# Kernel optimization log

Hardware: AMD Instinct MI355X
Metric: run time of the kernel (lower is better)

Reference implementation:

```python
import jax, jax.numpy as jnp
import numpy as np

DIM = 1024
N_HEADS = 16
HEAD_DIM = DIM // N_HEADS


def setup_inputs() -> dict:
    key = jax.random.key(0)
    ks = jax.random.split(key, 5)
    s = 0.02
    return {
        "x": jax.random.normal(ks[0], (2, 2048, DIM), dtype=jnp.float32),
        "w_qkv": jax.random.normal(ks[1], (DIM, 3 * DIM), dtype=jnp.float32) * s,
        "b_qkv": jnp.zeros((3 * DIM,), dtype=jnp.float32),
        "w_proj": jax.random.normal(ks[2], (DIM, DIM), dtype=jnp.float32) * s,
        "b_proj": jnp.zeros((DIM,), dtype=jnp.float32),
    }


def reference(x, w_qkv, b_qkv, w_proj, b_proj):
    B, N, C = x.shape
    H, D = N_HEADS, HEAD_DIM
    qkv = x @ w_qkv + b_qkv                      # [B, N, 3C]
    qkv = qkv.reshape(B, N, 3, H, D)
    q = qkv[:, :, 0].transpose(0, 2, 1, 3)       # [B, H, N, D]
    k = qkv[:, :, 1].transpose(0, 2, 1, 3)
    v = qkv[:, :, 2].transpose(0, 2, 1, 3)
    scale = 1.0 / np.sqrt(D).astype(np.float32)
    attn = jnp.einsum('bhnd,bhmd->bhnm', q, k) * scale
    attn = jax.nn.softmax(attn, axis=-1)
    out = jnp.einsum('bhnm,bhmd->bhnd', attn, v)  # [B, H, N, D]
    out = out.transpose(0, 2, 1, 3).reshape(B, N, C)
    return out @ w_proj + b_proj
```

## Files before the change

kernel.cpp:

```cpp
#include <hip/hip_runtime.h>

#define DIM    1024
#define NHEADS 16
#define HDIM   64
#define BATCH  2
#define SEQ    2048
#define ROWS   (BATCH * SEQ)
#define KDIM   1024

typedef __attribute__((ext_vector_type(4))) float f32x4;
typedef __attribute__((ext_vector_type(16))) float f32x16;
typedef __attribute__((ext_vector_type(8))) short bf16x8;

__device__ inline unsigned short f2bf(float f) {
  return (unsigned short)((__float_as_uint(f) + 0x8000u) >> 16);
}
__device__ inline float bf2f(unsigned short h) {
  return __uint_as_float(((unsigned int)h) << 16);
}
__device__ inline void split2(float x, unsigned short& hi, unsigned short& lo) {
  hi = f2bf(x);
  lo = f2bf(x - bf2f(hi));
}
__device__ inline int key2(int r) { return (r & 3) ^ ((r >> 2) & 3); }
__device__ inline int key8(int r) { return (r & 7) ^ ((r >> 3) & 7); }

__device__ inline void gll16(const void* g, void* lds_base) {
  __builtin_amdgcn_global_load_lds(
      (const __attribute__((address_space(1))) void*)g,
      (__attribute__((address_space(3))) void*)lds_base, 16, 0, 0);
}
__device__ inline unsigned int cvtpk_bf16(float a, float b) {
  unsigned int r;
  asm("v_cvt_pk_bf16_f32 %0, %1, %2" : "=v"(r) : "v"(a), "v"(b));
  return r;
}
template <int N>
__device__ inline void vm_wait() {
  if constexpr (N == 0)      asm volatile("s_waitcnt vmcnt(0)" ::: "memory");
  else if constexpr (N == 4) asm volatile("s_waitcnt vmcnt(4)" ::: "memory");
  else if constexpr (N == 6) asm volatile("s_waitcnt vmcnt(6)" ::: "memory");
  else                       asm volatile("s_waitcnt vmcnt(8)" ::: "memory");
}

__global__ __launch_bounds__(256) void split_x_kernel(
    const float* __restrict__ x, ushort* __restrict__ Xh) {
  const int i = blockIdx.x * 256 + threadIdx.x;
  const float4 v = ((const float4*)x)[i];
  ushort4 h4;
  h4.x = f2bf(v.x);
  h4.y = f2bf(v.y);
  h4.z = f2bf(v.z);
  h4.w = f2bf(v.w);
  ((ushort4*)Xh)[i] = h4;
}

template <int Ndim, bool LO>
__global__ __launch_bounds__(256) void tsplit_w(const float* __restrict__ W,
                                                ushort* __restrict__ WTh,
                                                ushort* __restrict__ WTl) {
  __shared__ float Ls[64][68];
  const int t = threadIdx.x;
  const int n0 = blockIdx.x * 64, k0 = blockIdx.y * 64;
#pragma unroll
  for (int pass = 0; pass < 4; ++pass) {
    const int kk = pass * 16 + (t >> 4);
    const float4 v =
        *(const float4*)(W + (size_t)(k0 + kk) * Ndim + n0 + (t & 15) * 4);
    *(float4*)&Ls[kk][(t & 15) * 4] = v;
  }
  __syncthreads();
  const int nloc = t >> 2, kc = (t & 3) * 16;
#pragma unroll
  for (int j = 0; j < 4; ++j) {
    ushort4 h4, l4;
    split2(Ls[kc + j * 4 + 0][nloc], h4.x, l4.x);
    split2(Ls[kc + j * 4 + 1][nloc], h4.y, l4.y);
    split2(Ls[kc + j * 4 + 2][nloc], h4.z, l4.z);
    split2(Ls[kc + j * 4 + 3][nloc], h4.w, l4.w);
    const size_t off = (size_t)(n0 + nloc) * KDIM + k0 + kc + j * 4;
    *(ushort4*)(WTh + off) = h4;
    if (LO) *(ushort4*)(WTl + off) = l4;
  }
}

template <int NPROD, int MODE, bool PIPE3>
__global__ __launch_bounds__(256) void gemm_mfma(
    const ushort* __restrict__ Ahp, const ushort* __restrict__ Alp,
    const ushort* __restrict__ Bhp, const ushort* __restrict__ Blp,
    const float* __restrict__ bias, float* __restrict__ Cout,
    ushort* __restrict__ Qh, ushort* __restrict__ Kh,
    ushort* __restrict__ VTh, int Ndim) {
  constexpr int NPLANES = NPROD + 1;
  constexpr int CALLS = NPLANES * 2;
  constexpr int BUFE = NPLANES * 128 * 32;
  constexpr int NBUF = PIPE3 ? 3 : 2;
  __shared__ ushort lds[NBUF][BUFE];

  const int t = threadIdx.x, w = t >> 6, lane = t & 63;
  const int l15 = lane & 15, lg = lane >> 4;
  const int n0 = blockIdx.x * 128, m0 = blockIdx.y * 128;
  const int wr = (w >> 1) * 64;
  const int wc = (w & 1) * 64;

  const ushort* srcs[4];
  srcs[0] = Ahp + (size_t)m0 * KDIM;
  if constexpr (NPROD == 1) {
    srcs[1] = Bhp + (size_t)n0 * KDIM;
    srcs[2] = srcs[3] = srcs[1];
  } else {
    srcs[1] = Alp + (size_t)m0 * KDIM;
    srcs[2] = Bhp + (size_t)n0 * KDIM;
    srcs[3] = Blp + (size_t)n0 * KDIM;
  }

  f32x4 acc[4][4];
#pragma unroll
  for (int a = 0; a < 4; ++a)
#pragma unroll
    for (int bq = 0; bq < 4; ++bq) acc[a][bq] = (f32x4){0.f, 0.f, 0.f, 0.f};

  auto stage = [&](int bi, int k0) {
#pragma unroll
    for (int i = 0; i < CALLS; ++i) {
      const int cbase = (w * CALLS + i) * 64;
      const int c = cbase + lane;
      const int p = c >> 9, cc = c & 511, r = cc >> 2, s = cc & 3;
      const ushort* g = srcs[p] + (size_t)r * KDIM + k0 + ((s ^ key2(r)) << 3);
      gll16(g, (char*)&lds[bi][0] + cbase * 16);
    }
  };

  auto compute = [&](const ushort* L) {
    if constexpr (NPROD == 1) {
      bf16x8 af[4];
#pragma unroll
      for (int mt = 0; mt < 4; ++mt) {
        const int row = wr + mt * 16 + l15;
        af[mt] = *(const bf16x8*)&L[row * 32 + ((lg ^ key2(row)) << 3)];
      }
      if constexpr (PIPE3) __builtin_amdgcn_s_setprio(1);
#pragma unroll
      for (int nt = 0; nt < 4; ++nt) {
        const int row = wc + nt * 16 + l15;
        const bf16x8 bh_ =
            *(const bf16x8*)&L[4096 + row * 32 + ((lg ^ key2(row)) << 3)];
#pragma unroll
        for (int mt = 0; mt < 4; ++mt)
          acc[mt][nt] = __builtin_amdgcn_mfma_f32_16x16x32_bf16(
              af[mt], bh_, acc[mt][nt], 0, 0, 0);
      }
      if constexpr (PIPE3) __builtin_amdgcn_s_setprio(0);
    } else {
      bf16x8 af[4][2];
#pragma unroll
      for (int mt = 0; mt < 4; ++mt) {
        const int row = wr + mt * 16 + l15;
        const int off = row * 32 + ((lg ^ key2(row)) << 3);
        af[mt][0] = *(const bf16x8*)&L[off];
        af[mt][1] = *(const bf16x8*)&L[4096 + off];
      }
      if constexpr (PIPE3) __builtin_amdgcn_s_setprio(1);
#pragma unroll
      for (int nt = 0; nt < 4; ++nt) {
        const int row = wc + nt * 16 + l15;
        const int off = row * 32 + ((lg ^ key2(row)) << 3);
        const bf16x8 bh_ = *(const bf16x8*)&L[8192 + off];
#pragma unroll
        for (int mt = 0; mt < 4; ++mt) {
          acc[mt][nt] = __builtin_amdgcn_mfma_f32_16x16x32_bf16(
              af[mt][0], bh_, acc[mt][nt], 0, 0, 0);
          acc[mt][nt] = __builtin_amdgcn_mfma_f32_16x16x32_bf16(
              af[mt][1], bh_, acc[mt][nt], 0, 0, 0);
        }
        const bf16x8 bl_ = *(const bf16x8*)&L[12288 + off];
#pragma unroll
        for (int mt = 0; mt < 4; ++mt)
          acc[mt][nt] = __builtin_amdgcn_mfma_f32_16x16x32_bf16(
              af[mt][0], bl_, acc[mt][nt], 0, 0, 0);
      }
      if constexpr (PIPE3) __builtin_amdgcn_s_setprio(0);
    }
  };

  if constexpr (PIPE3) {
    constexpr int NSTEP = KDIM / 32;
    stage(0, 0);
    stage(1, 32);
    for (int it = 0; it < NSTEP; ++it) {
      if (it + 1 < NSTEP) vm_wait<CALLS>(); else vm_wait<0>();
      __builtin_amdgcn_s_barrier();
      __builtin_amdgcn_sched_barrier(0);
      if (it + 2 < NSTEP) stage((it + 2) % 3, (it + 2) * 32);
      compute(&lds[it % 3][0]);
    }
  } else {
    stage(0, 0);
    __syncthreads();
    for (int k0 = 0, it = 0; k0 < KDIM; k0 += 32, ++it) {
      const int cur = it & 1;
      if (k0 + 32 < KDIM) stage(cur ^ 1, k0 + 32);
      compute(&lds[cur][0]);
      __syncthreads();
    }
  }

  if constexpr (MODE == 0) {
#pragma unroll
    for (int nt = 0; nt < 4; ++nt) {
      const int col = n0 + wc + nt * 16 + l15;
      const float bv = bias[col];
#pragma unroll
      for (int mt = 0; mt < 4; ++mt) {
        const int row = m0 + wr + mt * 16 + lg * 4;
#pragma unroll
        for (int r = 0; r < 4; ++r)
          Cout[(size_t)(row + r) * Ndim + col] = acc[mt][nt][r] + bv;
      }
    }
  } else {
    const int sec = n0 >> 10;
#pragma unroll
    for (int nt = 0; nt < 4; ++nt) {
      const int col = n0 + wc + nt * 16 + l15;
      const float bv = bias[col];
      const int cw = col & 1023;
      if (sec == 0) {
#pragma unroll
        for (int mt = 0; mt < 4; ++mt) {
          const int row = m0 + wr + mt * 16 + lg * 4;
#pragma unroll
          for (int r = 0; r < 4; ++r)
            Qh[(size_t)(row + r) * DIM + cw] =
                f2bf((acc[mt][nt][r] + bv) * (0.125f * 1.44269504f));
        }
      } else if (sec == 1) {
#pragma unroll
        for (int mt = 0; mt < 4; ++mt) {
          const int row = m0 + wr + mt * 16 + lg * 4;
#pragma unroll
          for (int r = 0; r < 4; ++r)
            Kh[(size_t)(row + r) * DIM + cw] = f2bf(acc[mt][nt][r] + bv);
        }
      } else {
        const int h = cw >> 6, d = cw & 63;
#pragma unroll
        for (int mt = 0; mt < 4; ++mt) {
          const int grow = m0 + wr + mt * 16 + lg * 4;
          const int b = grow >> 11, n = grow & 2047;
          ushort4 v4;
          v4.x = f2bf(acc[mt][nt][0] + bv);
          v4.y = f2bf(acc[mt][nt][1] + bv);
          v4.z = f2bf(acc[mt][nt][2] + bv);
          v4.w = f2bf(acc[mt][nt][3] + bv);
          *(ushort4*)(VTh + ((size_t)(b * NHEADS + h) * HDIM + d) * SEQ + n) =
              v4;
        }
      }
    }
  }
}

__global__ __launch_bounds__(256) void attn_mfma32(
    const ushort* __restrict__ Qhp, const ushort* __restrict__ Khp,
    const ushort* __restrict__ VThp, ushort* __restrict__ AOh,
    ushort* __restrict__ AOl) {
  __shared__ ushort KV2[3][2 * 64 * 64];

  const int t = threadIdx.x, w = t >> 6, lane = t & 63;
  const int l31 = lane & 31, hi = lane >> 5;
  const int q0 = blockIdx.x * 128;
  const int bh = blockIdx.y, b = bh >> 4, h = bh & 15;

  bf16x8 qf[4];
  {
    const ushort* qp = Qhp +
        (size_t)(b * SEQ + q0 + w * 32 + l31) * DIM + h * HDIM + hi * 8;
    int4 qi[4];
#pragma unroll
    for (int j = 0; j < 4; ++j) qi[j] = *(const int4*)(qp + 16 * j);
#pragma unroll
    for (int j = 0; j < 4; ++j) {
      asm volatile("" :: "v"(qi[j].x), "v"(qi[j].y), "v"(qi[j].z),
                   "v"(qi[j].w));
      qf[j] = __builtin_bit_cast(bf16x8, qi[j]);
    }
  }
  const ushort* kbase = Khp + (size_t)(b * SEQ) * DIM + h * HDIM;
  const ushort* vbase = VThp + (size_t)(b * NHEADS + h) * HDIM * SEQ;

  const bf16x8 vones = __builtin_bit_cast(
      bf16x8, (int4){0x3F803F80, 0x3F803F80, 0x3F803F80, 0x3F803F80});

  f32x16 o_[2];
  f32x16 o_l;
  o_[0] = f32x16{};
  o_[1] = f32x16{};
  o_l = f32x16{};

  auto stage = [&](int bi, int kt) {
    const int kv0 = kt * 64;
#pragma unroll
    for (int i = 0; i < 4; ++i) {
      const int cbase = (w * 4 + i) * 64;
      const int c = cbase + lane;
      const int p_ = c >> 9, cc = c & 511, r = cc >> 3, s = cc & 7;
      const ushort* g =
          (p_ == 0)
              ? kbase + (size_t)(kv0 + r) * DIM + ((s ^ key8(r)) << 3)
              : vbase + (size_t)r * SEQ + kv0 + ((s ^ key8(r)) << 3);
      gll16(g, (char*)&KV2[bi][0] + cbase * 16);
    }
  };

  constexpr int NT = SEQ / 64;
  stage(0, 0);
  stage(1, 1);

  for (int kt = 0; kt < NT; ++kt) {
    if (kt + 1 < NT) vm_wait<4>(); else vm_wait<0>();
    __builtin_amdgcn_s_barrier();
    __builtin_amdgcn_sched_barrier(0);
    if (kt + 2 < NT) stage((kt + 2) % 3, kt + 2);

    const ushort* Kt = &KV2[kt % 3][0];
    const ushort* Vt = &KV2[kt % 3][4096];

    f32x16 st[2];
    st[0] = f32x16{};
    st[1] = f32x16{};
    __builtin_amdgcn_s_setprio(1);
#pragma unroll
    for (int j = 0; j < 4; ++j) {
#pragma unroll
      for (int rb = 0; rb < 2; ++rb) {
        const int n = rb * 32 + l31;
        const bf16x8 kf =
            *(const bf16x8*)&Kt[n * 64 + (((2 * j + hi) ^ key8(n)) << 3)];
        st[rb] = __builtin_amdgcn_mfma_f32_32x32x16_bf16(kf, qf[j], st[rb],
                                                         0, 0, 0);
      }
    }
    __builtin_amdgcn_s_setprio(0);

    unsigned int u[2][8];
#pragma unroll
    for (int rb = 0; rb < 2; ++rb) {
      float p[16];
#pragma unroll
      for (int r = 0; r < 16; ++r) p[r] = __builtin_amdgcn_exp2f(st[rb][r]);
#pragma unroll
      for (int j = 0; j < 8; ++j) u[rb][j] = cvtpk_bf16(p[2 * j], p[2 * j + 1]);
    }

    __builtin_amdgcn_s_setprio(1);
#pragma unroll
    for (int kc = 0; kc < 4; ++kc) {
      const unsigned int* ub = &u[kc >> 1][4 * (kc & 1)];
      const bf16x8 pa = __builtin_bit_cast(
          bf16x8, (int4){(int)ub[0], (int)ub[1], (int)ub[2], (int)ub[3]});
      o_l = __builtin_amdgcn_mfma_f32_32x32x16_bf16(pa, vones, o_l, 0, 0, 0);
#pragma unroll
      for (int dblk = 0; dblk < 2; ++dblk) {
        const int d = dblk * 32 + l31;
        const int rowoff = d * 64;
        const int k8d = key8(d);
        const int2 va = *(const int2*)&Vt[rowoff + (((2 * kc) ^ k8d) << 3) +
                                          4 * hi];
        const int2 vb = *(const int2*)&Vt[rowoff +
                                          (((2 * kc + 1) ^ k8d) << 3) + 4 * hi];
        const bf16x8 vf =
            __builtin_bit_cast(bf16x8, (int4){va.x, va.y, vb.x, vb.y});
        o_[dblk] = __builtin_amdgcn_mfma_f32_32x32x16_bf16(pa, vf, o_[dblk],
                                                           0, 0, 0);
      }
    }
    __builtin_amdgcn_s_setprio(0);
  }

  float inv[16];
#pragma unroll
  for (int r = 0; r < 16; ++r) inv[r] = 1.0f / o_l[r];

#pragma unroll
  for (int dblk = 0; dblk < 2; ++dblk)
#pragma unroll
    for (int r = 0; r < 16; ++r) {
      const int q = q0 + w * 32 + (r & 3) + 8 * (r >> 2) + 4 * hi;
      unsigned short hi16, lo16;
      split2(o_[dblk][r] * inv[r], hi16, lo16);
      const size_t off =
          (size_t)(b * SEQ + q) * DIM + h * HDIM + dblk * 32 + l31;
      AOh[off] = hi16;
      AOl[off] = lo16;
    }
}

extern "C" void kernel_launch(void* const* d_in, const int* in_sizes, int n_in,
                              void* d_out, int out_size, void* d_ws,
                              size_t ws_size, hipStream_t stream) {
  const float* x      = (const float*)d_in[0];
  const float* w_qkv  = (const float*)d_in[1];
  const float* b_qkv  = (const float*)d_in[2];
  const float* w_proj = (const float*)d_in[3];
  const float* b_proj = (const float*)d_in[4];
  float* out = (float*)d_out;

  ushort* p = (ushort*)d_ws;
  ushort* WqT_h = p;  p += (size_t)3072 * 1024;
  ushort* WpT_h = p;  p += (size_t)1024 * 1024;
  ushort* WpT_l = p;  p += (size_t)1024 * 1024;
  ushort* Xh    = p;  p += (size_t)ROWS * 1024;
  ushort* Xl    = p;  p += (size_t)ROWS * 1024;
  ushort* Qh    = p;  p += (size_t)ROWS * 1024;
  ushort* Kh    = p;  p += (size_t)ROWS * 1024;
  ushort* VTh   = p;  p += (size_t)ROWS * 1024;
  ushort* AOh = Xh;
  ushort* AOl = Xl;

  split_x_kernel<<<ROWS * DIM / 4 / 256, 256, 0, stream>>>(x, Xh);
  tsplit_w<3072, false>
      <<<dim3(48, 16), 256, 0, stream>>>(w_qkv, WqT_h, nullptr);
  tsplit_w<1024, true>
      <<<dim3(16, 16), 256, 0, stream>>>(w_proj, WpT_h, WpT_l);

  gemm_mfma<1, 1, false><<<dim3(24, 32), 256, 0, stream>>>(
      Xh, nullptr, WqT_h, nullptr, b_qkv, nullptr, Qh, Kh, VTh, 3072);

  attn_mfma32<<<dim3(SEQ / 128, BATCH * NHEADS), 256, 0, stream>>>(
      Qh, Kh, VTh, AOh, AOl);

  gemm_mfma<3, 0, true><<<dim3(8, 32), 256, 0, stream>>>(
      AOh, AOl, WpT_h, WpT_l, b_proj, out, nullptr, nullptr, nullptr, 1024);
}
```

Measured before the change: 138.8 us.

## Split attention KV range across two blocks and merge with a combine kernel

The attention grid is doubled so each block processes half of the key/value sequence. The first split writes unnormalized fp32 partial outputs and the second writes bf16 hi/lo partials, both alongside per-row sums. A new combine kernel adds the partials and normalizes by the summed denominators. This aims to raise occupancy and parallelism across CUs. In exchange it adds an extra launch and extra global memory traffic, and it shrinks the shared-memory pipeline from triple to double buffering with a full wait each tile.

Result: slower. 149.2 us, median of 3 (+7.5%).

```diff
diff --git a/kernel.cpp b/kernel.cpp
--- a/kernel.cpp
+++ b/kernel.cpp
@@ -263,14 +263,16 @@
 
 __global__ __launch_bounds__(256) void attn_mfma32(
     const ushort* __restrict__ Qhp, const ushort* __restrict__ Khp,
-    const ushort* __restrict__ VThp, ushort* __restrict__ AOh,
+    const ushort* __restrict__ VThp, float* __restrict__ Opf,
+    float* __restrict__ Lsum, ushort* __restrict__ AOh,
     ushort* __restrict__ AOl) {
-  __shared__ ushort KV2[3][2 * 64 * 64];
+  __shared__ ushort KV2[2][2 * 64 * 64];
 
   const int t = threadIdx.x, w = t >> 6, lane = t & 63;
   const int l31 = lane & 31, hi = lane >> 5;
   const int q0 = blockIdx.x * 128;
-  const int bh = blockIdx.y, b = bh >> 4, h = bh & 15;
+  const int bh = blockIdx.y & 31, split = blockIdx.y >> 5;
+  const int b = bh >> 4, h = bh & 15;
 
   bf16x8 qf[4];
   {
@@ -298,8 +300,8 @@
   o_[1] = f32x16{};
   o_l = f32x16{};
 
-  auto stage = [&](int bi, int kt) {
-    const int kv0 = kt * 64;
+  auto stage = [&](int bi, int ktile) {
+    const int kv0 = ktile * 64;
 #pragma unroll
     for (int i = 0; i < 4; ++i) {
       const int cbase = (w * 4 + i) * 64;
@@ -313,18 +315,18 @@
     }
   };
 
-  constexpr int NT = SEQ / 64;
-  stage(0, 0);
-  stage(1, 1);
-
-  for (int kt = 0; kt < NT; ++kt) {
-    if (kt + 1 < NT) vm_wait<4>(); else vm_wait<0>();
+  constexpr int NT2 = SEQ / 64 / 2;
+  const int tb = split * NT2;
+  stage(0, tb);
+
+  for (int kt = 0; kt < NT2; ++kt) {
+    vm_wait<0>();
     __builtin_amdgcn_s_barrier();
     __builtin_amdgcn_sched_barrier(0);
-    if (kt + 2 < NT) stage((kt + 2) % 3, kt + 2);
-
-    const ushort* Kt = &KV2[kt % 3][0];
-    const ushort* Vt = &KV2[kt % 3][4096];
+    if (kt + 1 < NT2) stage((kt + 1) & 1, tb + kt + 1);
+
+    const ushort* Kt = &KV2[kt & 1][0];
+    const ushort* Vt = &KV2[kt & 1][4096];
 
     f32x16 st[2];
     st[0] = f32x16{};
@@ -378,22 +380,60 @@
     __builtin_amdgcn_s_setprio(0);
   }
 
-  float inv[16];
-#pragma unroll
-  for (int r = 0; r < 16; ++r) inv[r] = 1.0f / o_l[r];
-
 #pragma unroll
   for (int dblk = 0; dblk < 2; ++dblk)
 #pragma unroll
     for (int r = 0; r < 16; ++r) {
       const int q = q0 + w * 32 + (r & 3) + 8 * (r >> 2) + 4 * hi;
-      unsigned short hi16, lo16;
-      split2(o_[dblk][r] * inv[r], hi16, lo16);
       const size_t off =
           (size_t)(b * SEQ + q) * DIM + h * HDIM + dblk * 32 + l31;
-      AOh[off] = hi16;
-      AOl[off] = lo16;
-    }
+      if (split == 0) {
+        Opf[off] = o_[dblk][r];
+      } else {
+        unsigned short hi16, lo16;
+        split2(o_[dblk][r], hi16, lo16);
+        AOh[off] = hi16;
+        AOl[off] = lo16;
+      }
+    }
+  if (l31 == 0) {
+#pragma unroll
+    for (int r = 0; r < 16; ++r) {
+      const int q = q0 + w * 32 + (r & 3) + 8 * (r >> 2) + 4 * hi;
+      Lsum[split * (32 * SEQ) + bh * SEQ + q] = o_l[r];
+    }
+  }
+}
+
+__global__ __launch_bounds__(256) void combine_kernel(
+    const float* __restrict__ Opf, const float* __restrict__ Lsum,
+    ushort* __restrict__ AOh, ushort* __restrict__ AOl) {
+  const size_t i0 = ((size_t)blockIdx.x * 256 + threadIdx.x) * 8;
+  const int row = (int)(i0 >> 10), col = (int)(i0 & 1023);
+  const int b = row >> 11, n = row & 2047, h = col >> 6;
+  const int li = (b * NHEADS + h) * SEQ + n;
+  const float inv = 1.0f / (Lsum[li] + Lsum[32 * SEQ + li]);
+
+  const float4 o0a = *(const float4*)(Opf + i0);
+  const float4 o0b = *(const float4*)(Opf + i0 + 4);
+  ushort4 ha = *(const ushort4*)(AOh + i0);
+  ushort4 hb = *(const ushort4*)(AOh + i0 + 4);
+  ushort4 la = *(const ushort4*)(AOl + i0);
+  ushort4 lb = *(const ushort4*)(AOl + i0 + 4);
+
+  float o0[8] = {o0a.x, o0a.y, o0a.z, o0a.w, o0b.x, o0b.y, o0b.z, o0b.w};
+  unsigned short hs[8] = {ha.x, ha.y, ha.z, ha.w, hb.x, hb.y, hb.z, hb.w};
+  unsigned short ls[8] = {la.x, la.y, la.z, la.w, lb.x, lb.y, lb.z, lb.w};
+#pragma unroll
+  for (int e = 0; e < 8; ++e) {
+    const float v1 = bf2f(hs[e]) + bf2f(ls[e]);
+    const float o = (o0[e] + v1) * inv;
+    split2(o, hs[e], ls[e]);
+  }
+  *(ushort4*)(AOh + i0) = (ushort4){hs[0], hs[1], hs[2], hs[3]};
+  *(ushort4*)(AOh + i0 + 4) = (ushort4){hs[4], hs[5], hs[6], hs[7]};
+  *(ushort4*)(AOl + i0) = (ushort4){ls[0], ls[1], ls[2], ls[3]};
+  *(ushort4*)(AOl + i0 + 4) = (ushort4){ls[4], ls[5], ls[6], ls[7]};
 }
 
 extern "C" void kernel_launch(void* const* d_in, const int* in_sizes, int n_in,
@@ -415,6 +455,8 @@
   ushort* Qh    = p;  p += (size_t)ROWS * 1024;
   ushort* Kh    = p;  p += (size_t)ROWS * 1024;
   ushort* VTh   = p;  p += (size_t)ROWS * 1024;
+  float* Opf    = (float*)p;  p += (size_t)ROWS * 1024 * 2;
+  float* Lsum   = (float*)p;  p += (size_t)2 * 32 * SEQ * 2;
   ushort* AOh = Xh;
   ushort* AOl = Xl;
 
@@ -427,8 +469,11 @@
   gemm_mfma<1, 1, false><<<dim3(24, 32), 256, 0, stream>>>(
       Xh, nullptr, WqT_h, nullptr, b_qkv, nullptr, Qh, Kh, VTh, 3072);
 
-  attn_mfma32<<<dim3(SEQ / 128, BATCH * NHEADS), 256, 0, stream>>>(
-      Qh, Kh, VTh, AOh, AOl);
+  attn_mfma32<<<dim3(SEQ / 128, 64), 256, 0, stream>>>(
+      Qh, Kh, VTh, Opf, Lsum, AOh, AOl);
+
+  combine_kernel<<<dim3(ROWS * DIM / (256 * 8)), 256, 0, stream>>>(
+      Opf, Lsum, AOh, AOl);
 
   gemm_mfma<3, 0, true><<<dim3(8, 32), 256, 0, stream>>>(
       AOh, AOl, WpT_h, WpT_l, b_proj, out, nullptr, nullptr, nullptr, 1024);
```
